# Optimization experiments

Hardware: AMD Instinct MI355X
Metric: run time of the kernel (lower is better)

## Reference

```python
import jax, jax.numpy as jnp
import numpy as np

NUM_CQ = 16
NUM_CODES = 8192
NUM_SAMPLES = 16
TEMP = 1.0
NHEADS = 4
DM = 32
EMB = 768
B, L = 64, 512


def setup_inputs():
    key = jax.random.key(0)
    ks = jax.random.split(key, 16)

    def lin(k, shape):
        fan_in = shape[-1]
        return (jax.random.uniform(k, shape, jnp.float32, -1.0, 1.0) / np.sqrt(fan_in)).astype(jnp.float32)

    xcq = jax.random.normal(ks[0], (B, L, EMB), jnp.float32)
    attn_mask = jax.random.randint(ks[1], (B, L - NUM_CQ), 0, 2, dtype=jnp.int32)
    cb = jax.random.normal(ks[2], (NUM_CODES, EMB), jnp.float32)
    codebook = 100.0 * cb / jnp.linalg.norm(cb, axis=-1, keepdims=True)  # matches 100*normalize init
    return dict(
        xcq=xcq, attn_mask=attn_mask,
        fc_in_w=lin(ks[3], (DM, EMB)), fc_in_b=jnp.zeros((DM,), jnp.float32),
        fc_out_w=lin(ks[4], (EMB, DM)), fc_out_b=jnp.zeros((EMB,), jnp.float32),
        enc_in_w=lin(ks[5], (2, 3 * DM, DM)), enc_in_b=jnp.zeros((2, 3 * DM), jnp.float32),
        enc_out_w=lin(ks[6], (2, DM, DM)), enc_out_b=jnp.zeros((2, DM), jnp.float32),
        enc_ff1_w=lin(ks[7], (2, 2 * DM, DM)), enc_ff1_b=jnp.zeros((2, 2 * DM), jnp.float32),
        enc_ff2_w=lin(ks[8], (2, DM, 2 * DM)), enc_ff2_b=jnp.zeros((2, DM), jnp.float32),
        enc_ln1_g=jnp.ones((2, DM), jnp.float32), enc_ln1_b=jnp.zeros((2, DM), jnp.float32),
        enc_ln2_g=jnp.ones((2, DM), jnp.float32), enc_ln2_b=jnp.zeros((2, DM), jnp.float32),
        codebook=codebook,
    )


def _layernorm(x, g, b):
    mu = jnp.mean(x, -1, keepdims=True)
    var = jnp.mean((x - mu) ** 2, -1, keepdims=True)
    return g * (x - mu) / jnp.sqrt(var + 1e-5) + b


def _forward(xcq, attn_mask, fc_in_w, fc_in_b, fc_out_w, fc_out_b,
             enc_in_w, enc_in_b, enc_out_w, enc_out_b,
             enc_ff1_w, enc_ff1_b, enc_ff2_w, enc_ff2_b,
             enc_ln1_g, enc_ln1_b, enc_ln2_g, enc_ln2_b, codebook):
    Bb, Ll, _ = xcq.shape
    dh = DM // NHEADS
    x = xcq @ fc_in_w.T + fc_in_b  # [B, L, 32]
    # ones for the cq tokens, then the provided mask; True = valid key
    valid = jnp.concatenate([jnp.ones((Bb, NUM_CQ), bool), attn_mask.astype(bool)], axis=1)  # [B, L]
    for l in range(2):  # torch post-norm TransformerEncoderLayer, relu, dropout=0 (eval)
        qkv = x @ enc_in_w[l].T + enc_in_b[l]
        q, k, v = jnp.split(qkv, 3, axis=-1)
        sh = lambda t: t.reshape(Bb, Ll, NHEADS, dh).transpose(0, 2, 1, 3)  # [B,h,L,dh]
        q, k, v = sh(q), sh(k), sh(v)
        scores = jnp.einsum('bhqd,bhkd->bhqk', q, k) / np.sqrt(dh)
        scores = jnp.where(valid[:, None, None, :], scores, -1e9)  # key padding mask
        attn = jax.nn.softmax(scores, axis=-1)
        o = jnp.einsum('bhqk,bhkd->bhqd', attn, v).transpose(0, 2, 1, 3).reshape(Bb, Ll, DM)
        o = o @ enc_out_w[l].T + enc_out_b[l]
        x = _layernorm(x + o, enc_ln1_g[l], enc_ln1_b[l])
        h = jax.nn.relu(x @ enc_ff1_w[l].T + enc_ff1_b[l]) @ enc_ff2_w[l].T + enc_ff2_b[l]
        x = _layernorm(x + h, enc_ln2_g[l], enc_ln2_b[l])
    xc_out = x[:, :NUM_CQ] @ fc_out_w.T + fc_out_b  # [B, ncq, 768]
    flat = xc_out.reshape(-1, EMB)  # [N, 768]
    dists = (jnp.sum(flat ** 2, 1, keepdims=True) + jnp.sum(codebook ** 2, 1)
             - 2.0 * (flat @ codebook.T))  # [N, K] squared euclidean
    logits = (-dists - 1e-5) / TEMP
    N = Bb * NUM_CQ
    # multinomial(total_count=NUM_SAMPLES): draw S categoricals per row and count
    draws = jax.random.categorical(jax.random.key(42), logits, shape=(NUM_SAMPLES, N))  # [S, N]
    rows = jnp.broadcast_to(jnp.arange(N), (NUM_SAMPLES, N))
    samples = jnp.zeros((N, NUM_CODES), jnp.float32).at[rows, draws].add(1.0)  # [N, K] counts
    xq = (samples @ codebook).reshape(xc_out.shape) / NUM_SAMPLES
    xc_quantized = xc_out + jax.lax.stop_gradient(xq - xc_out)  # straight-through estimator
    return xc_quantized


def reference(xcq, attn_mask, fc_in_w, fc_in_b, fc_out_w, fc_out_b,
              enc_in_w, enc_in_b, enc_out_w, enc_out_b,
              enc_ff1_w, enc_ff1_b, enc_ff2_w, enc_ff2_b,
              enc_ln1_g, enc_ln1_b, enc_ln2_g, enc_ln2_b, codebook):
    xc_quantized = _forward(xcq, attn_mask, fc_in_w, fc_in_b, fc_out_w, fc_out_b,
                            enc_in_w, enc_in_b, enc_out_w, enc_out_b,
                            enc_ff1_w, enc_ff1_b, enc_ff2_w, enc_ff2_b,
                            enc_ln1_g, enc_ln1_b, enc_ln2_g, enc_ln2_b, codebook)
    return (xc_quantized, xcq)
```

## Files before the change

### kernel.cpp

```cpp
#include <hip/hip_runtime.h>
#include <stdint.h>

#define NCODES 8192
#define NROWS 1024

#define OFF_LOGITS 0ll
#define OFF_X      8388608ll
#define OFF_QKV    9437184ll
#define OFF_ATTN   12582912ll
#define OFF_FLAT   13631488ll
#define OFF_CSQ    14418944ll

__device__ __forceinline__ uint32_t rotl32(uint32_t x, int r) { return (x << r) | (x >> (32 - r)); }

__device__ __forceinline__ void tf2x32_key42(uint32_t x0, uint32_t x1, uint32_t& o0, uint32_t& o1) {
  const uint32_t k0 = 0u, k1 = 42u;
  const uint32_t k2 = k0 ^ k1 ^ 0x1BD11BDAu;
  x0 += k0; x1 += k1;
  x0 += x1; x1 = rotl32(x1,13); x1 ^= x0;
  x0 += x1; x1 = rotl32(x1,15); x1 ^= x0;
  x0 += x1; x1 = rotl32(x1,26); x1 ^= x0;
  x0 += x1; x1 = rotl32(x1, 6); x1 ^= x0;
  x0 += k1; x1 += k2 + 1u;
  x0 += x1; x1 = rotl32(x1,17); x1 ^= x0;
  x0 += x1; x1 = rotl32(x1,29); x1 ^= x0;
  x0 += x1; x1 = rotl32(x1,16); x1 ^= x0;
  x0 += x1; x1 = rotl32(x1,24); x1 ^= x0;
  x0 += k2; x1 += k0 + 2u;
  x0 += x1; x1 = rotl32(x1,13); x1 ^= x0;
  x0 += x1; x1 = rotl32(x1,15); x1 ^= x0;
  x0 += x1; x1 = rotl32(x1,26); x1 ^= x0;
  x0 += x1; x1 = rotl32(x1, 6); x1 ^= x0;
  x0 += k0; x1 += k1 + 3u;
  x0 += x1; x1 = rotl32(x1,17); x1 ^= x0;
  x0 += x1; x1 = rotl32(x1,29); x1 ^= x0;
  x0 += x1; x1 = rotl32(x1,16); x1 ^= x0;
  x0 += x1; x1 = rotl32(x1,24); x1 ^= x0;
  x0 += k1; x1 += k2 + 4u;
  x0 += x1; x1 = rotl32(x1,13); x1 ^= x0;
  x0 += x1; x1 = rotl32(x1,15); x1 ^= x0;
  x0 += x1; x1 = rotl32(x1,26); x1 ^= x0;
  x0 += x1; x1 = rotl32(x1, 6); x1 ^= x0;
  x0 += k2; x1 += k0 + 5u;
  o0 = x0; o1 = x1;
}

__device__ __forceinline__ float gumbel_at(uint32_t idx) {
  uint32_t y0, y1;
  tf2x32_key42(0u, idx, y0, y1);
  uint32_t bits = y0 ^ y1;
  float f = __uint_as_float((bits >> 9) | 0x3f800000u) - 1.0f;
  float u = fmaxf(f, 1.17549435e-38f);
  return -logf(-logf(u));
}

__global__ __launch_bounds__(256) void k_fcin(const float* __restrict__ xcq,
                                              const float* __restrict__ W,
                                              const float* __restrict__ b,
                                              float* __restrict__ x,
                                              float* __restrict__ outcopy) {
  __shared__ float xs[64 * 36];
  int t = threadIdx.x;
  int w = t >> 6, lane = t & 63;
  long tb = (long)blockIdx.x * 64;
  const float4* xcq4 = (const float4*)xcq;
  float4* out4 = (float4*)outcopy;
  const float4* W4 = (const float4*)W;
  float acc[8];
  #pragma unroll
  for (int i = 0; i < 8; i++) acc[i] = 0.f;

  for (int jc4 = 0; jc4 < 192; jc4 += 8) {
    __syncthreads();
    #pragma unroll
    for (int p = 0; p < 2; p++) {
      int f = t + 256 * p;
      int row = f >> 3, j4 = f & 7;
      long g = (tb + row) * 192 + jc4 + j4;
      float4 v = xcq4[g];
      *(float4*)(xs + row * 36 + j4 * 4) = v;
      out4[g] = v;
    }
    __syncthreads();
    #pragma unroll
    for (int j4 = 0; j4 < 8; j4++) {
      float4 xv = *(const float4*)(xs + lane * 36 + j4 * 4);
      #pragma unroll
      for (int ci = 0; ci < 8; ci++) {
        int c = w * 8 + ci;
        float4 wv = W4[c * 192 + jc4 + j4];
        acc[ci] += xv.x * wv.x + xv.y * wv.y + xv.z * wv.z + xv.w * wv.w;
      }
    }
  }
  __syncthreads();
  *(float4*)(xs + lane * 36 + w * 8)     = make_float4(acc[0] + b[w*8+0], acc[1] + b[w*8+1], acc[2] + b[w*8+2], acc[3] + b[w*8+3]);
  *(float4*)(xs + lane * 36 + w * 8 + 4) = make_float4(acc[4] + b[w*8+4], acc[5] + b[w*8+5], acc[6] + b[w*8+6], acc[7] + b[w*8+7]);
  __syncthreads();
  float4* x4 = (float4*)x;
  #pragma unroll
  for (int p = 0; p < 2; p++) {
    int f = t + 256 * p;
    int row = f >> 3, c4 = f & 7;
    x4[(tb + row) * 8 + c4] = *(const float4*)(xs + row * 36 + c4 * 4);
  }
}

__global__ __launch_bounds__(64) void k_qkv(const float* __restrict__ x,
                                            const float* __restrict__ W,
                                            const float* __restrict__ b,
                                            float* __restrict__ qkv) {
  long token = (long)blockIdx.x * 64 + threadIdx.x;
  const float4* x4 = (const float4*)x;
  const float4* W4 = (const float4*)W;
  float4* q4 = (float4*)qkv;
  float4 xr[8];
  #pragma unroll
  for (int j4 = 0; j4 < 8; j4++) xr[j4] = x4[token * 8 + j4];
  #pragma unroll
  for (int c4 = 0; c4 < 24; c4++) {
    float s[4];
    #pragma unroll
    for (int q = 0; q < 4; q++) {
      int c = c4 * 4 + q;
      float acc = 0.f;
      #pragma unroll
      for (int j4 = 0; j4 < 8; j4++) {
        float4 wv = W4[c * 8 + j4];
        acc += xr[j4].x * wv.x + xr[j4].y * wv.y + xr[j4].z * wv.z + xr[j4].w * wv.w;
      }
      s[q] = acc + b[c];
    }
    q4[token * 24 + c4] = make_float4(s[0], s[1], s[2], s[3]);
  }
}

__global__ __launch_bounds__(256) void k_attn(const float* __restrict__ qkv,
                                              const int* __restrict__ amask,
                                              float* __restrict__ attno) {
  int z = blockIdx.x;
  int b = z >> 3;
  int h = (z >> 1) & 3;
  int half = z & 1;
  __shared__ float4 ks4[512 * 2];
  __shared__ float4 vs4[512 * 2];
  __shared__ float inval[512];
  int t = threadIdx.x;
  long qb4 = (long)b * 512 * 24;
  const float4* qkv4 = (const float4*)qkv;
  #pragma unroll
  for (int p = 0; p < 4; p++) {
    int f = t + 256 * p;
    int tok = f >> 1, hf = f & 1;
    ks4[f] = qkv4[qb4 + (long)tok * 24 + 8 + h * 2 + hf];
    vs4[f] = qkv4[qb4 + (long)tok * 24 + 16 + h * 2 + hf];
  }
  #pragma unroll
  for (int p = 0; p < 2; p++) {
    int l = t + 256 * p;
    inval[l] = (l < 16 || amask[b * 496 + (l - 16)] != 0) ? 0.f : 1.f;
  }
  __syncthreads();
  const float scale = 0.35355339059327373f;
  int lq = half * 256 + t;
  float4 qa = qkv4[qb4 + (long)lq * 24 + h * 2];
  float4 qb = qkv4[qb4 + (long)lq * 24 + h * 2 + 1];
  float m = -3.4e38f;
  for (int lk = 0; lk < 512; lk++) {
    float4 ka = ks4[lk * 2], kb = ks4[lk * 2 + 1];
    float s = qa.x*ka.x + qa.y*ka.y + qa.z*ka.z + qa.w*ka.w
            + qb.x*kb.x + qb.y*kb.y + qb.z*kb.z + qb.w*kb.w;
    s *= scale;
    s = inval[lk] != 0.f ? -1e9f : s;
    m = fmaxf(m, s);
  }
  float denom = 0.f;
  float4 o0 = make_float4(0,0,0,0), o1 = make_float4(0,0,0,0);
  for (int lk = 0; lk < 512; lk++) {
    float4 ka = ks4[lk * 2], kb = ks4[lk * 2 + 1];
    float s = qa.x*ka.x + qa.y*ka.y + qa.z*ka.z + qa.w*ka.w
            + qb.x*kb.x + qb.y*kb.y + qb.z*kb.z + qb.w*kb.w;
    s *= scale;
    s = inval[lk] != 0.f ? -1e9f : s;
    float p = expf(s - m);
    denom += p;
    float4 va = vs4[lk * 2], vb = vs4[lk * 2 + 1];
    o0.x += p * va.x; o0.y += p * va.y; o0.z += p * va.z; o0.w += p * va.w;
    o1.x += p * vb.x; o1.y += p * vb.y; o1.z += p * vb.z; o1.w += p * vb.w;
  }
  float inv = 1.f / denom;
  float4* a4 = (float4*)attno;
  long ob = ((long)b * 512 + lq) * 8 + h * 2;
  a4[ob]     = make_float4(o0.x*inv, o0.y*inv, o0.z*inv, o0.w*inv);
  a4[ob + 1] = make_float4(o1.x*inv, o1.y*inv, o1.z*inv, o1.w*inv);
}

__global__ __launch_bounds__(64) void k_oproj_ln(const float* __restrict__ attno,
                                                 const float* __restrict__ W,
                                                 const float* __restrict__ b,
                                                 const float* __restrict__ g,
                                                 const float* __restrict__ beta,
                                                 float* __restrict__ x) {
  long token = (long)blockIdx.x * 64 + threadIdx.x;
  const float4* a4 = (const float4*)attno;
  const float4* x4 = (const float4*)x;
  const float4* W4 = (const float4*)W;
  float4 orow[8];
  float xr[32];
  #pragma unroll
  for (int j4 = 0; j4 < 8; j4++) {
    orow[j4] = a4[token * 8 + j4];
    float4 v = x4[token * 8 + j4];
    xr[j4*4] = v.x; xr[j4*4+1] = v.y; xr[j4*4+2] = v.z; xr[j4*4+3] = v.w;
  }
  float v[32];
  #pragma unroll
  for (int c = 0; c < 32; c++) {
    float acc = 0.f;
    #pragma unroll
    for (int j4 = 0; j4 < 8; j4++) {
      float4 wv = W4[c * 8 + j4];
      acc += orow[j4].x * wv.x + orow[j4].y * wv.y + orow[j4].z * wv.z + orow[j4].w * wv.w;
    }
    v[c] = acc + b[c] + xr[c];
  }
  float mu = 0.f;
  #pragma unroll
  for (int c = 0; c < 32; c++) mu += v[c];
  mu *= 0.03125f;
  float var = 0.f;
  #pragma unroll
  for (int c = 0; c < 32; c++) { float d = v[c] - mu; var += d * d; }
  var *= 0.03125f;
  float inv = 1.f / sqrtf(var + 1e-5f);
  float4* xo4 = (float4*)x;
  #pragma unroll
  for (int j4 = 0; j4 < 8; j4++) {
    float4 o;
    o.x = g[j4*4]   * (v[j4*4]   - mu) * inv + beta[j4*4];
    o.y = g[j4*4+1] * (v[j4*4+1] - mu) * inv + beta[j4*4+1];
    o.z = g[j4*4+2] * (v[j4*4+2] - mu) * inv + beta[j4*4+2];
    o.w = g[j4*4+3] * (v[j4*4+3] - mu) * inv + beta[j4*4+3];
    xo4[token * 8 + j4] = o;
  }
}

__global__ __launch_bounds__(64) void k_ffn_ln(const float* __restrict__ x,
                                               const float* __restrict__ W1,
                                               const float* __restrict__ b1,
                                               const float* __restrict__ W2,
                                               const float* __restrict__ b2,
                                               const float* __restrict__ g,
                                               const float* __restrict__ beta,
                                               float* __restrict__ xout) {
  long token = (long)blockIdx.x * 64 + threadIdx.x;
  const float4* x4 = (const float4*)x;
  const float4* W14 = (const float4*)W1;
  const float4* W24 = (const float4*)W2;
  float xr[32];
  #pragma unroll
  for (int j4 = 0; j4 < 8; j4++) {
    float4 v = x4[token * 8 + j4];
    xr[j4*4] = v.x; xr[j4*4+1] = v.y; xr[j4*4+2] = v.z; xr[j4*4+3] = v.w;
  }
  float h[64];
  #pragma unroll
  for (int c = 0; c < 64; c++) {
    float acc = 0.f;
    #pragma unroll
    for (int j4 = 0; j4 < 8; j4++) {
      float4 wv = W14[c * 8 + j4];
      acc += xr[j4*4] * wv.x + xr[j4*4+1] * wv.y + xr[j4*4+2] * wv.z + xr[j4*4+3] * wv.w;
    }
    h[c] = fmaxf(acc + b1[c], 0.f);
  }
  float v[32];
  #pragma unroll
  for (int c = 0; c < 32; c++) {
    float acc = 0.f;
    #pragma unroll
    for (int j4 = 0; j4 < 16; j4++) {
      float4 wv = W24[c * 16 + j4];
      acc += h[j4*4] * wv.x + h[j4*4+1] * wv.y + h[j4*4+2] * wv.z + h[j4*4+3] * wv.w;
    }
    v[c] = acc + b2[c] + xr[c];
  }
  float mu = 0.f;
  #pragma unroll
  for (int c = 0; c < 32; c++) mu += v[c];
  mu *= 0.03125f;
  float var = 0.f;
  #pragma unroll
  for (int c = 0; c < 32; c++) { float d = v[c] - mu; var += d * d; }
  var *= 0.03125f;
  float inv = 1.f / sqrtf(var + 1e-5f);
  float4* xo4 = (float4*)xout;
  #pragma unroll
  for (int j4 = 0; j4 < 8; j4++) {
    float4 o;
    o.x = g[j4*4]   * (v[j4*4]   - mu) * inv + beta[j4*4];
    o.y = g[j4*4+1] * (v[j4*4+1] - mu) * inv + beta[j4*4+1];
    o.z = g[j4*4+2] * (v[j4*4+2] - mu) * inv + beta[j4*4+2];
    o.w = g[j4*4+3] * (v[j4*4+3] - mu) * inv + beta[j4*4+3];
    xo4[token * 8 + j4] = o;
  }
}

__global__ __launch_bounds__(256) void k_fcout(const float* __restrict__ x,
                                               const float* __restrict__ W,
                                               const float* __restrict__ b,
                                               float* __restrict__ flat) {
  int bb = blockIdx.x;
  __shared__ float xs[16 * 32];
  int t = threadIdx.x;
  if (t < 128) {
    int row = t >> 3, j4 = t & 7;
    *(float4*)(xs + row * 32 + j4 * 4) =
        *(const float4*)(x + ((long)bb * 512 + row) * 32 + j4 * 4);
  }
  __syncthreads();
  #pragma unroll
  for (int i = 0; i < 3; i++) {
    int e = t + 256 * i;
    const float4* w4 = (const float4*)(W + e * 32);
    float4 wv[8];
    #pragma unroll
    for (int j4 = 0; j4 < 8; j4++) wv[j4] = w4[j4];
    float bias = b[e];
    #pragma unroll
    for (int r = 0; r < 16; r++) {
      float s = 0.f;
      #pragma unroll
      for (int j4 = 0; j4 < 8; j4++) {
        const float* xr = xs + r * 32 + j4 * 4;
        s += xr[0] * wv[j4].x + xr[1] * wv[j4].y + xr[2] * wv[j4].z + xr[3] * wv[j4].w;
      }
      flat[((long)bb * 16 + r) * 768 + e] = s + bias;
    }
  }
}

__global__ __launch_bounds__(256) void k_cbsq(const float* __restrict__ cb,
                                              float* __restrict__ cb_sq) {
  int w = threadIdx.x >> 6, lane = threadIdx.x & 63;
  int k = blockIdx.x * 4 + w;
  const float* row = cb + (long)k * 768;
  float s = 0.f;
  #pragma unroll
  for (int i = 0; i < 12; i++) { float v = row[lane + 64 * i]; s += v * v; }
  #pragma unroll
  for (int off = 32; off >= 1; off >>= 1) s += __shfl_xor(s, off);
  if (lane == 0) cb_sq[k] = s;
}

__device__ __forceinline__ ushort f2bf(float x) {
  uint32_t u = __float_as_uint(x);
  uint32_t r = (u + 0x7fffu + ((u >> 16) & 1u)) >> 16;
  return (ushort)r;
}

__global__ __launch_bounds__(256) void k_tobf16(const float* __restrict__ src,
                                                ushort* __restrict__ dst, long n4) {
  long i = (long)blockIdx.x * 256 + threadIdx.x;
  if (i >= n4) return;
  float4 v = ((const float4*)src)[i];
  ushort4 o;
  o.x = f2bf(v.x); o.y = f2bf(v.y); o.z = f2bf(v.z); o.w = f2bf(v.w);
  ((ushort4*)dst)[i] = o;
}

typedef __attribute__((ext_vector_type(8))) short bf16x8;
typedef __attribute__((ext_vector_type(4))) float f32x4;

__global__ __launch_bounds__(256, 2) void k_logits_mfma(const ushort* __restrict__ fbf,
                                                        const ushort* __restrict__ cbbf,
                                                        float* __restrict__ approx) {
  __shared__ __align__(16) short As[128 * 64];
  __shared__ __align__(16) short Bs[128 * 64];
  int t = threadIdx.x;
  int mb = blockIdx.x & 7;
  int nb = blockIdx.x >> 3;
  int w = t >> 6, lane = t & 63;
  int wr = w >> 1, wc = w & 1;

  f32x4 zero; zero.x = 0.f; zero.y = 0.f; zero.z = 0.f; zero.w = 0.f;
  f32x4 acc[4][4];
  #pragma unroll
  for (int i = 0; i < 4; i++)
    #pragma unroll
    for (int j = 0; j < 4; j++) acc[i][j] = zero;

  for (int kt = 0; kt < 12; kt++) {
    int kc = kt * 64;
    bf16x8 ra[4], rb[4];
    #pragma unroll
    for (int p = 0; p < 4; p++) {
      int li = p * 256 + t;
      int row = li >> 3, s = li & 7;
      ra[p] = *(const bf16x8*)(fbf + (long)(mb * 128 + row) * 768 + kc + s * 8);
      rb[p] = *(const bf16x8*)(cbbf + (long)(nb * 128 + row) * 768 + kc + s * 8);
    }
    __syncthreads();
    #pragma unroll
    for (int p = 0; p < 4; p++) {
      int li = p * 256 + t;
      int row = li >> 3, s = li & 7, ss = s ^ (row & 7);
      *(bf16x8*)(As + row * 64 + ss * 8) = ra[p];
      *(bf16x8*)(Bs + row * 64 + ss * 8) = rb[p];
    }
    __syncthreads();
    #pragma unroll
    for (int ks = 0; ks < 2; ks++) {
      int slot = ks * 4 + (lane >> 4);
      bf16x8 a[4], b[4];
      #pragma unroll
      for (int i = 0; i < 4; i++) {
        int rowa = wr * 64 + i * 16 + (lane & 15);
        a[i] = *(const bf16x8*)(As + rowa * 64 + (slot ^ (rowa & 7)) * 8);
        int rowb = wc * 64 + i * 16 + (lane & 15);
        b[i] = *(const bf16x8*)(Bs + rowb * 64 + (slot ^ (rowb & 7)) * 8);
      }
      #pragma unroll
      for (int i = 0; i < 4; i++)
        #pragma unroll
        for (int j = 0; j < 4; j++)
          acc[i][j] = __builtin_amdgcn_mfma_f32_16x16x32_bf16(a[i], b[j], acc[i][j], 0, 0, 0);
    }
  }
  long rbase = (long)mb * 128 + wr * 64 + (lane >> 4) * 4;
  int cbase = nb * 128 + wc * 64 + (lane & 15);
  #pragma unroll
  for (int i = 0; i < 4; i++) {
    #pragma unroll
    for (int j = 0; j < 4; j++) {
      f32x4 v = acc[i][j];
      long r0 = rbase + i * 16;
      int c = cbase + j * 16;
      approx[(r0 + 0) * 8192 + c] = 2.f * v.x;
      approx[(r0 + 1) * 8192 + c] = 2.f * v.y;
      approx[(r0 + 2) * 8192 + c] = 2.f * v.z;
      approx[(r0 + 3) * 8192 + c] = 2.f * v.w;
    }
  }
}

__global__ __launch_bounds__(256) void k_sample(const float* __restrict__ approx,
                                                const float* __restrict__ cb,
                                                const float* __restrict__ csq,
                                                const float* __restrict__ flat,
                                                float* __restrict__ out0) {
  int n = blockIdx.x, t = threadIdx.x;
  const float* arow = approx + (long)n * 8192;
  __shared__ float s_max[4];
  __shared__ int s_cnt;
  __shared__ int cand[8192];
  __shared__ float fs[768];
  __shared__ float redv[64];
  __shared__ int redi[64];
  __shared__ int draws[16];
  if (t < 192) ((float4*)fs)[t] = ((const float4*)(flat + (long)n * 768))[t];
  float va[32];
  float m = -3.4e38f;
  #pragma unroll
  for (int i = 0; i < 32; i++) { va[i] = arow[t + 256 * i]; m = fmaxf(m, va[i]); }
  #pragma unroll
  for (int off = 32; off >= 1; off >>= 1) m = fmaxf(m, __shfl_xor(m, off));
  if ((t & 63) == 0) s_max[t >> 6] = m;
  if (t == 0) s_cnt = 0;
  __syncthreads();
  float rowmax = fmaxf(fmaxf(s_max[0], s_max[1]), fmaxf(s_max[2], s_max[3]));
  float thresh = rowmax - 30.0f;
  #pragma unroll
  for (int i = 0; i < 32; i++) {
    if (va[i] >= thresh) { int p = atomicAdd(&s_cnt, 1); cand[p] = t + 256 * i; }
  }
  __syncthreads();
  int ncand = s_cnt;
  float bv[16]; int bi[16];
  #pragma unroll
  for (int s = 0; s < 16; s++) { bv[s] = -3.4e38f; bi[s] = 0x7fffffff; }
  for (int c = t; c < ncand; c += 256) {
    int k = cand[c];
    const float4* cb4 = (const float4*)(cb + (long)k * 768);
    float acc = 0.f;
    #pragma unroll 8
    for (int j4 = 0; j4 < 192; j4++) {
      float4 wv = cb4[j4];
      const float* xr = fs + j4 * 4;
      acc = fmaf(xr[0], wv.x, acc);
      acc = fmaf(xr[1], wv.y, acc);
      acc = fmaf(xr[2], wv.z, acc);
      acc = fmaf(xr[3], wv.w, acc);
    }
    float lg = 2.f * acc - csq[k] - 1e-5f;
    #pragma unroll
    for (int s = 0; s < 16; s++) {
      uint32_t idx = ((uint32_t)((s << 10) + n) << 13) | (uint32_t)k;
      float val = gumbel_at(idx) + lg;
      if (val > bv[s] || (val == bv[s] && k < bi[s])) { bv[s] = val; bi[s] = k; }
    }
  }
  #pragma unroll
  for (int s = 0; s < 16; s++) {
    #pragma unroll
    for (int off = 32; off >= 1; off >>= 1) {
      float ov = __shfl_xor(bv[s], off);
      int oi = __shfl_xor(bi[s], off);
      if (ov > bv[s] || (ov == bv[s] && oi < bi[s])) { bv[s] = ov; bi[s] = oi; }
    }
    if ((t & 63) == 0) { redv[s * 4 + (t >> 6)] = bv[s]; redi[s * 4 + (t >> 6)] = bi[s]; }
  }
  __syncthreads();
  if (t < 16) {
    float bvv = redv[t * 4]; int bii = redi[t * 4];
    #pragma unroll
    for (int w = 1; w < 4; w++) {
      float ov = redv[t * 4 + w]; int oi = redi[t * 4 + w];
      if (ov > bvv || (ov == bvv && oi < bii)) { bvv = ov; bii = oi; }
    }
    draws[t] = bii;
  }
  __syncthreads();
  #pragma unroll
  for (int i = 0; i < 3; i++) {
    int e = t + 256 * i;
    float ssum = 0.f;
    #pragma unroll
    for (int s = 0; s < 16; s++) ssum += cb[(long)draws[s] * 768 + e];
    float xq = ssum * 0.0625f;
    float fl = fs[e];
    out0[(long)n * 768 + e] = fl + (xq - fl);
  }
}

extern "C" void kernel_launch(void* const* d_in, const int* in_sizes, int n_in,
                              void* d_out, int out_size, void* d_ws, size_t ws_size,
                              hipStream_t stream) {
  (void)in_sizes; (void)n_in; (void)out_size; (void)ws_size;
  const float* xcq      = (const float*)d_in[0];
  const int*   amask    = (const int*)d_in[1];
  const float* fc_in_w  = (const float*)d_in[2];
  const float* fc_in_b  = (const float*)d_in[3];
  const float* fc_out_w = (const float*)d_in[4];
  const float* fc_out_b = (const float*)d_in[5];
  const float* enc_in_w = (const float*)d_in[6];
  const float* enc_in_b = (const float*)d_in[7];
  const float* enc_out_w= (const float*)d_in[8];
  const float* enc_out_b= (const float*)d_in[9];
  const float* ff1w     = (const float*)d_in[10];
  const float* ff1b     = (const float*)d_in[11];
  const float* ff2w     = (const float*)d_in[12];
  const float* ff2b     = (const float*)d_in[13];
  const float* ln1g     = (const float*)d_in[14];
  const float* ln1b     = (const float*)d_in[15];
  const float* ln2g     = (const float*)d_in[16];
  const float* ln2b     = (const float*)d_in[17];
  const float* cb       = (const float*)d_in[18];
  float* out = (float*)d_out;
  float* ws  = (float*)d_ws;

  float* x      = ws + OFF_X;
  float* qkv    = ws + OFF_QKV;
  float* attno  = ws + OFF_ATTN;
  float* flat   = ws + OFF_FLAT;
  float* csq    = ws + OFF_CSQ;
  float* approx = ws + OFF_LOGITS;
  ushort* cbbf  = (ushort*)(ws + OFF_QKV);
  ushort* fbf   = (ushort*)(ws + OFF_ATTN);

  k_fcin<<<512, 256, 0, stream>>>(xcq, fc_in_w, fc_in_b, x, out + 786432);
  for (int l = 0; l < 2; l++) {
    k_qkv<<<512, 64, 0, stream>>>(x, enc_in_w + l * 96 * 32, enc_in_b + l * 96, qkv);
    k_attn<<<512, 256, 0, stream>>>(qkv, amask, attno);
    k_oproj_ln<<<512, 64, 0, stream>>>(attno, enc_out_w + l * 32 * 32, enc_out_b + l * 32,
                                       ln1g + l * 32, ln1b + l * 32, x);
    k_ffn_ln<<<512, 64, 0, stream>>>(x, ff1w + l * 64 * 32, ff1b + l * 64,
                                     ff2w + l * 32 * 64, ff2b + l * 32,
                                     ln2g + l * 32, ln2b + l * 32, x);
  }
  k_fcout<<<64, 256, 0, stream>>>(x, fc_out_w, fc_out_b, flat);
  k_cbsq<<<2048, 256, 0, stream>>>(cb, csq);
  k_tobf16<<<6144, 256, 0, stream>>>(cb, cbbf, 1572864ll);
  k_tobf16<<<768, 256, 0, stream>>>(flat, fbf, 196608ll);
  k_logits_mfma<<<512, 256, 0, stream>>>(fbf, cbbf, approx);
  k_sample<<<1024, 256, 0, stream>>>(approx, cb, csq, flat, out);
}
```

Baseline: 984.4 us.

## Double-buffer fc_in input tiles with direct global-to-LDS loads and XOR swizzle

Rewrites the fc_in projection kernel so each K-tile of xcq is loaded straight into LDS with global_load_lds, into two alternating buffers. The next tile's load is issued before computing on the current one. The LDS layout changes from padded rows to an XOR-swizzled layout to avoid bank conflicts. The output copy of xcq is now written from LDS instead of from registers. The aim is to overlap the streaming load of the large input with compute and to drop one barrier per tile. It relies on the builtin's wave-uniform LDS addressing and on waits being correctly placed before the barrier.

```diff
diff --git a/kernel.cpp b/kernel.cpp
--- a/kernel.cpp
+++ b/kernel.cpp
@@ -59,50 +59,64 @@
                                               const float* __restrict__ b,
                                               float* __restrict__ x,
                                               float* __restrict__ outcopy) {
-  __shared__ float xs[64 * 36];
+  __shared__ __align__(16) float xs[2][64 * 32];
   int t = threadIdx.x;
   int w = t >> 6, lane = t & 63;
   long tb = (long)blockIdx.x * 64;
-  const float4* xcq4 = (const float4*)xcq;
+  const float4* W4 = (const float4*)W;
   float4* out4 = (float4*)outcopy;
-  const float4* W4 = (const float4*)W;
   float acc[8];
   #pragma unroll
   for (int i = 0; i < 8; i++) acc[i] = 0.f;
 
-  for (int jc4 = 0; jc4 < 192; jc4 += 8) {
+  #define STAGE(kt, buf)                                                              \
+    {                                                                                 \
+      _Pragma("unroll")                                                               \
+      for (int q = 0; q < 2; q++) {                                                   \
+        int p = w * 128 + q * 64 + lane;                                              \
+        int row = p >> 3;                                                             \
+        int srcslot = (p & 7) ^ (row & 7);                                            \
+        const float* g = xcq + ((tb + row) * 192 + (kt) * 8 + srcslot) * 4;           \
+        __builtin_amdgcn_global_load_lds(                                             \
+            (const __attribute__((address_space(1))) uint32_t*)g,                     \
+            (__attribute__((address_space(3))) uint32_t*)&xs[buf][p * 4], 16, 0, 0);  \
+      }                                                                               \
+    }
+
+  STAGE(0, 0);
+  for (int kt = 0; kt < 24; kt++) {
     __syncthreads();
+    if (kt < 23) STAGE(kt + 1, (kt + 1) & 1);
+    const float* cur = xs[kt & 1];
+    #pragma unroll
+    for (int j4 = 0; j4 < 8; j4++) {
+      float4 xv = *(const float4*)(cur + (lane * 8 + (j4 ^ (lane & 7))) * 4);
+      #pragma unroll
+      for (int ci = 0; ci < 8; ci++) {
+        float4 wv = W4[(w * 8 + ci) * 192 + kt * 8 + j4];
+        acc[ci] += xv.x * wv.x + xv.y * wv.y + xv.z * wv.z + xv.w * wv.w;
+      }
+    }
     #pragma unroll
     for (int p = 0; p < 2; p++) {
       int f = t + 256 * p;
-      int row = f >> 3, j4 = f & 7;
-      long g = (tb + row) * 192 + jc4 + j4;
-      float4 v = xcq4[g];
-      *(float4*)(xs + row * 36 + j4 * 4) = v;
-      out4[g] = v;
-    }
-    __syncthreads();
-    #pragma unroll
-    for (int j4 = 0; j4 < 8; j4++) {
-      float4 xv = *(const float4*)(xs + lane * 36 + j4 * 4);
-      #pragma unroll
-      for (int ci = 0; ci < 8; ci++) {
-        int c = w * 8 + ci;
-        float4 wv = W4[c * 192 + jc4 + j4];
-        acc[ci] += xv.x * wv.x + xv.y * wv.y + xv.z * wv.z + xv.w * wv.w;
-      }
-    }
-  }
-  __syncthreads();
-  *(float4*)(xs + lane * 36 + w * 8)     = make_float4(acc[0] + b[w*8+0], acc[1] + b[w*8+1], acc[2] + b[w*8+2], acc[3] + b[w*8+3]);
-  *(float4*)(xs + lane * 36 + w * 8 + 4) = make_float4(acc[4] + b[w*8+4], acc[5] + b[w*8+5], acc[6] + b[w*8+6], acc[7] + b[w*8+7]);
+      int row = f >> 3, slot = f & 7;
+      float4 v = *(const float4*)(cur + (row * 8 + (slot ^ (row & 7))) * 4);
+      out4[(tb + row) * 192 + kt * 8 + slot] = v;
+    }
+  }
+  #undef STAGE
+  __syncthreads();
+  float* xsf = xs[0];
+  *(float4*)(xsf + lane * 32 + w * 8)     = make_float4(acc[0] + b[w*8+0], acc[1] + b[w*8+1], acc[2] + b[w*8+2], acc[3] + b[w*8+3]);
+  *(float4*)(xsf + lane * 32 + w * 8 + 4) = make_float4(acc[4] + b[w*8+4], acc[5] + b[w*8+5], acc[6] + b[w*8+6], acc[7] + b[w*8+7]);
   __syncthreads();
   float4* x4 = (float4*)x;
   #pragma unroll
   for (int p = 0; p < 2; p++) {
     int f = t + 256 * p;
     int row = f >> 3, c4 = f & 7;
-    x4[(tb + row) * 8 + c4] = *(const float4*)(xs + row * 36 + c4 * 4);
+    x4[(tb + row) * 8 + c4] = *(const float4*)(xsf + row * 32 + c4 * 4);
   }
 }
 
```

New measurement: 977.1 us. Within noise of the previous version (-0.7%).

## Double-buffer fc_in with direct global-to-LDS loads; process two queries per attention thread

Applied to the files above, without the earlier changes.

The fc_in kernel now streams xcq into a double-buffered, XOR-swizzled LDS tile using global_load_lds with explicit vmcnt waits. This overlaps the loads with compute and cuts the number of barriers. The output copy of xcq is written from LDS rather than from registers. Separately, each attention thread now handles two query rows, so every K/V LDS read is reused twice, and the grid is halved to 256 blocks. The cost is more LDS per block (64 KB) and fewer attention blocks, which may lower occupancy and parallelism.

```diff
diff --git a/kernel.cpp b/kernel.cpp
--- a/kernel.cpp
+++ b/kernel.cpp
@@ -59,50 +59,77 @@
                                               const float* __restrict__ b,
                                               float* __restrict__ x,
                                               float* __restrict__ outcopy) {
-  __shared__ float xs[64 * 36];
+  __shared__ __align__(16) float xs[2][64 * 128];
   int t = threadIdx.x;
   int w = t >> 6, lane = t & 63;
+  int wu = __builtin_amdgcn_readfirstlane(w);
   long tb = (long)blockIdx.x * 64;
-  const float4* xcq4 = (const float4*)xcq;
+  const float4* W4 = (const float4*)W;
   float4* out4 = (float4*)outcopy;
-  const float4* W4 = (const float4*)W;
   float acc[8];
   #pragma unroll
   for (int i = 0; i < 8; i++) acc[i] = 0.f;
 
-  for (int jc4 = 0; jc4 < 192; jc4 += 8) {
-    __syncthreads();
-    #pragma unroll
-    for (int p = 0; p < 2; p++) {
-      int f = t + 256 * p;
-      int row = f >> 3, j4 = f & 7;
-      long g = (tb + row) * 192 + jc4 + j4;
-      float4 v = xcq4[g];
-      *(float4*)(xs + row * 36 + j4 * 4) = v;
-      out4[g] = v;
-    }
-    __syncthreads();
-    #pragma unroll
-    for (int j4 = 0; j4 < 8; j4++) {
-      float4 xv = *(const float4*)(xs + lane * 36 + j4 * 4);
-      #pragma unroll
-      for (int ci = 0; ci < 8; ci++) {
-        int c = w * 8 + ci;
-        float4 wv = W4[c * 192 + jc4 + j4];
-        acc[ci] += xv.x * wv.x + xv.y * wv.y + xv.z * wv.z + xv.w * wv.w;
-      }
-    }
-  }
-  __syncthreads();
-  *(float4*)(xs + lane * 36 + w * 8)     = make_float4(acc[0] + b[w*8+0], acc[1] + b[w*8+1], acc[2] + b[w*8+2], acc[3] + b[w*8+3]);
-  *(float4*)(xs + lane * 36 + w * 8 + 4) = make_float4(acc[4] + b[w*8+4], acc[5] + b[w*8+5], acc[6] + b[w*8+6], acc[7] + b[w*8+7]);
+#define STAGE(kt, buf)                                                               \
+  { _Pragma("unroll")                                                                \
+    for (int q = 0; q < 8; q++) {                                                    \
+      int p = (w * 8 + q) * 64 + lane;                                               \
+      int row = p >> 5, sl = p & 31;                                                 \
+      int sls = (sl & ~7) | ((sl & 7) ^ (row & 7));                                  \
+      const float* g = xcq + ((tb + row) * 192 + (kt) * 32 + sls) * 4;               \
+      __builtin_amdgcn_global_load_lds(                                              \
+          (const __attribute__((address_space(1))) uint32_t*)g,                      \
+          (__attribute__((address_space(3))) uint32_t*)&xs[buf][p * 4], 16, 0, 0);   \
+    } }
+
+#define COMPUTE(kt, buf)                                                             \
+  { _Pragma("unroll")                                                                \
+    for (int j4 = 0; j4 < 32; j4++) {                                                \
+      int ph = (j4 & ~7) | ((j4 & 7) ^ (lane & 7));                                  \
+      float4 xv = *(const float4*)(&xs[buf][(lane * 32 + ph) * 4]);                  \
+      _Pragma("unroll")                                                              \
+      for (int ci = 0; ci < 8; ci++) {                                               \
+        float4 wv = W4[(wu * 8 + ci) * 192 + (kt) * 32 + j4];            \
+        acc[ci] += xv.x * wv.x + xv.y * wv.y + xv.z * wv.z + xv.w * wv.w;            \
+      } } }
+
+#define COPYOUT(kt, buf)                                                             \
+  { int row = t >> 2, g0 = (t & 3) * 8;                                              \
+    _Pragma("unroll")                                                                \
+    for (int i = 0; i < 8; i++) {                                                    \
+      int ph = g0 + (i ^ (row & 7));                                                 \
+      float4 v = *(const float4*)(&xs[buf][(row * 32 + ph) * 4]);                    \
+      out4[(tb + row) * 192 + (kt) * 32 + g0 + i] = v;                               \
+    } }
+
+#define WAITV(N) asm volatile("s_waitcnt vmcnt(" #N ")" ::: "memory")
+#define CFENCE() asm volatile("" ::: "memory")
+#define BAR() __builtin_amdgcn_s_barrier()
+
+  STAGE(0, 0);
+  STAGE(1, 1); WAITV(8);  BAR(); COMPUTE(0, 0); COPYOUT(0, 0); CFENCE(); BAR();
+  STAGE(2, 0); WAITV(16); BAR(); COMPUTE(1, 1); COPYOUT(1, 1); CFENCE(); BAR();
+  STAGE(3, 1); WAITV(16); BAR(); COMPUTE(2, 0); COPYOUT(2, 0); CFENCE(); BAR();
+  STAGE(4, 0); WAITV(16); BAR(); COMPUTE(3, 1); COPYOUT(3, 1); CFENCE(); BAR();
+  STAGE(5, 1); WAITV(16); BAR(); COMPUTE(4, 0); COPYOUT(4, 0); CFENCE(); BAR();
+               WAITV(8);  BAR(); COMPUTE(5, 1); COPYOUT(5, 1); CFENCE();
+#undef STAGE
+#undef COMPUTE
+#undef COPYOUT
+#undef WAITV
+#undef CFENCE
+#undef BAR
+  __syncthreads();
+  float* xsf = xs[0];
+  *(float4*)(xsf + lane * 36 + w * 8)     = make_float4(acc[0] + b[w*8+0], acc[1] + b[w*8+1], acc[2] + b[w*8+2], acc[3] + b[w*8+3]);
+  *(float4*)(xsf + lane * 36 + w * 8 + 4) = make_float4(acc[4] + b[w*8+4], acc[5] + b[w*8+5], acc[6] + b[w*8+6], acc[7] + b[w*8+7]);
   __syncthreads();
   float4* x4 = (float4*)x;
   #pragma unroll
   for (int p = 0; p < 2; p++) {
     int f = t + 256 * p;
     int row = f >> 3, c4 = f & 7;
-    x4[(tb + row) * 8 + c4] = *(const float4*)(xs + row * 36 + c4 * 4);
+    x4[(tb + row) * 8 + c4] = *(const float4*)(xsf + row * 36 + c4 * 4);
   }
 }
 
@@ -139,9 +166,8 @@
                                               const int* __restrict__ amask,
                                               float* __restrict__ attno) {
   int z = blockIdx.x;
-  int b = z >> 3;
-  int h = (z >> 1) & 3;
-  int half = z & 1;
+  int b = z >> 2;
+  int h = z & 3;
   __shared__ float4 ks4[512 * 2];
   __shared__ float4 vs4[512 * 2];
   __shared__ float inval[512];
@@ -162,37 +188,60 @@
   }
   __syncthreads();
   const float scale = 0.35355339059327373f;
-  int lq = half * 256 + t;
-  float4 qa = qkv4[qb4 + (long)lq * 24 + h * 2];
-  float4 qb = qkv4[qb4 + (long)lq * 24 + h * 2 + 1];
-  float m = -3.4e38f;
+  float4 qa0 = qkv4[qb4 + (long)t * 24 + h * 2];
+  float4 qb0 = qkv4[qb4 + (long)t * 24 + h * 2 + 1];
+  float4 qa1 = qkv4[qb4 + (long)(t + 256) * 24 + h * 2];
+  float4 qb1 = qkv4[qb4 + (long)(t + 256) * 24 + h * 2 + 1];
+  float m0 = -3.4e38f, m1 = -3.4e38f;
+  #pragma unroll 2
   for (int lk = 0; lk < 512; lk++) {
     float4 ka = ks4[lk * 2], kb = ks4[lk * 2 + 1];
-    float s = qa.x*ka.x + qa.y*ka.y + qa.z*ka.z + qa.w*ka.w
-            + qb.x*kb.x + qb.y*kb.y + qb.z*kb.z + qb.w*kb.w;
-    s *= scale;
-    s = inval[lk] != 0.f ? -1e9f : s;
-    m = fmaxf(m, s);
-  }
-  float denom = 0.f;
-  float4 o0 = make_float4(0,0,0,0), o1 = make_float4(0,0,0,0);
+    float iv = inval[lk];
+    float s0 = qa0.x*ka.x + qa0.y*ka.y + qa0.z*ka.z + qa0.w*ka.w
+             + qb0.x*kb.x + qb0.y*kb.y + qb0.z*kb.z + qb0.w*kb.w;
+    s0 *= scale;
+    s0 = iv != 0.f ? -1e9f : s0;
+    m0 = fmaxf(m0, s0);
+    float s1 = qa1.x*ka.x + qa1.y*ka.y + qa1.z*ka.z + qa1.w*ka.w
+             + qb1.x*kb.x + qb1.y*kb.y + qb1.z*kb.z + qb1.w*kb.w;
+    s1 *= scale;
+    s1 = iv != 0.f ? -1e9f : s1;
+    m1 = fmaxf(m1, s1);
+  }
+  float d0 = 0.f, d1 = 0.f;
+  float4 o00 = make_float4(0,0,0,0), o01 = make_float4(0,0,0,0);
+  float4 o10 = make_float4(0,0,0,0), o11 = make_float4(0,0,0,0);
+  #pragma unroll 2
   for (int lk = 0; lk < 512; lk++) {
     float4 ka = ks4[lk * 2], kb = ks4[lk * 2 + 1];
-    float s = qa.x*ka.x + qa.y*ka.y + qa.z*ka.z + qa.w*ka.w
-            + qb.x*kb.x + qb.y*kb.y + qb.z*kb.z + qb.w*kb.w;
-    s *= scale;
-    s = inval[lk] != 0.f ? -1e9f : s;
-    float p = expf(s - m);
-    denom += p;
     float4 va = vs4[lk * 2], vb = vs4[lk * 2 + 1];
-    o0.x += p * va.x; o0.y += p * va.y; o0.z += p * va.z; o0.w += p * va.w;
-    o1.x += p * vb.x; o1.y += p * vb.y; o1.z += p * vb.z; o1.w += p * vb.w;
-  }
-  float inv = 1.f / denom;
+    float iv = inval[lk];
+    float s0 = qa0.x*ka.x + qa0.y*ka.y + qa0.z*ka.z + qa0.w*ka.w
+             + qb0.x*kb.x + qb0.y*kb.y + qb0.z*kb.z + qb0.w*kb.w;
+    s0 *= scale;
+    s0 = iv != 0.f ? -1e9f : s0;
+    float p0 = expf(s0 - m0);
+    d0 += p0;
+    o00.x += p0 * va.x; o00.y += p0 * va.y; o00.z += p0 * va.z; o00.w += p0 * va.w;
+    o01.x += p0 * vb.x; o01.y += p0 * vb.y; o01.z += p0 * vb.z; o01.w += p0 * vb.w;
+    float s1 = qa1.x*ka.x + qa1.y*ka.y + qa1.z*ka.z + qa1.w*ka.w
+             + qb1.x*kb.x + qb1.y*kb.y + qb1.z*kb.z + qb1.w*kb.w;
+    s1 *= scale;
+    s1 = iv != 0.f ? -1e9f : s1;
+    float p1 = expf(s1 - m1);
+    d1 += p1;
+    o10.x += p1 * va.x; o10.y += p1 * va.y; o10.z += p1 * va.z; o10.w += p1 * va.w;
+    o11.x += p1 * vb.x; o11.y += p1 * vb.y; o11.z += p1 * vb.z; o11.w += p1 * vb.w;
+  }
   float4* a4 = (float4*)attno;
-  long ob = ((long)b * 512 + lq) * 8 + h * 2;
-  a4[ob]     = make_float4(o0.x*inv, o0.y*inv, o0.z*inv, o0.w*inv);
-  a4[ob + 1] = make_float4(o1.x*inv, o1.y*inv, o1.z*inv, o1.w*inv);
+  float inv0 = 1.f / d0;
+  long ob0 = ((long)b * 512 + t) * 8 + h * 2;
+  a4[ob0]     = make_float4(o00.x*inv0, o00.y*inv0, o00.z*inv0, o00.w*inv0);
+  a4[ob0 + 1] = make_float4(o01.x*inv0, o01.y*inv0, o01.z*inv0, o01.w*inv0);
+  float inv1 = 1.f / d1;
+  long ob1 = ((long)b * 512 + t + 256) * 8 + h * 2;
+  a4[ob1]     = make_float4(o10.x*inv1, o10.y*inv1, o10.z*inv1, o10.w*inv1);
+  a4[ob1 + 1] = make_float4(o11.x*inv1, o11.y*inv1, o11.z*inv1, o11.w*inv1);
 }
 
 __global__ __launch_bounds__(64) void k_oproj_ln(const float* __restrict__ attno,
@@ -571,7 +620,7 @@
   k_fcin<<<512, 256, 0, stream>>>(xcq, fc_in_w, fc_in_b, x, out + 786432);
   for (int l = 0; l < 2; l++) {
     k_qkv<<<512, 64, 0, stream>>>(x, enc_in_w + l * 96 * 32, enc_in_b + l * 96, qkv);
-    k_attn<<<512, 256, 0, stream>>>(qkv, amask, attno);
+    k_attn<<<256, 256, 0, stream>>>(qkv, amask, attno);
     k_oproj_ln<<<512, 64, 0, stream>>>(attno, enc_out_w + l * 32 * 32, enc_out_b + l * 32,
                                        ln1g + l * 32, ln1b + l * 32, x);
     k_ffn_ln<<<512, 64, 0, stream>>>(x, ff1w + l * 64 * 32, ff1b + l * 64,
```

After: 1.031 ms. 4.8% more time.
